# Performance work log

Hardware: AMD Instinct MI355X
Metric: run time of the kernel (lower is better)

Reference implementation:

```python
import math
import jax, jax.numpy as jnp
import numpy as np

N_HEADS = 16


def setup_inputs() -> dict:
    key = jax.random.key(0)
    qkv = jax.random.normal(key, (4, 3072, 2048), dtype=jnp.float32)
    return {"qkv": qkv}


def reference(qkv) -> jnp.ndarray:
    bs, width, length = qkv.shape
    assert width % (3 * N_HEADS) == 0
    ch = width // (3 * N_HEADS)
    # [bs*H, 3*ch, T] -> q, k, v each [bs*H, ch, T]
    qkv_r = qkv.reshape(bs * N_HEADS, 3 * ch, length)
    q, k, v = qkv_r[:, :ch], qkv_r[:, ch:2 * ch], qkv_r[:, 2 * ch:]
    scale = 1.0 / math.sqrt(math.sqrt(ch))
    # scores: [bs*H, T, T]
    weight = jnp.einsum('bct,bcs->bts', q * scale, k * scale)
    weight = jax.nn.softmax(weight.astype(jnp.float32), axis=-1).astype(weight.dtype)
    a = jnp.einsum('bts,bcs->bct', weight, v)  # [bs*H, ch, T]
    return a.reshape(bs, N_HEADS * ch, length)
```

## Files before the change

### kernel.cpp

```cpp
#include <hip/hip_runtime.h>
#include <hip/hip_bf16.h>
#include <cstdint>
#include <cstddef>

typedef short bf16x8 __attribute__((ext_vector_type(8)));
typedef float f32x16 __attribute__((ext_vector_type(16)));
typedef unsigned int uint2v __attribute__((ext_vector_type(2)));

#if __has_builtin(__builtin_amdgcn_exp2f)
#define EXP2F(x) __builtin_amdgcn_exp2f(x)
#else
#define EXP2F(x) exp2f(x)
#endif

#define QSCALE 0.18033688011112043f

__device__ __forceinline__ short f2bf(float f) {
  union { __hip_bfloat16 b; short s; } u;
  u.b = __float2bfloat16(f);
  return u.s;
}

__device__ __forceinline__ unsigned int fbits(float f) {
  union { float f; unsigned int u; } x; x.f = f; return x.u;
}
__device__ __forceinline__ float bfloat(unsigned int u) {
  union { unsigned int u; float f; } x; x.u = u; return x.f;
}

__device__ __forceinline__ unsigned int pkbf(float a, float b) {
  return ((fbits(a) + 0x8000u) >> 16) | ((fbits(b) + 0x8000u) & 0xFFFF0000u);
}

__device__ __forceinline__ float fmax_x32(float v) {
  const uint2v r = __builtin_amdgcn_permlane32_swap(fbits(v), fbits(v),
                                                    false, false);
  return fmaxf(bfloat(r[0]), bfloat(r[1]));
}
__device__ __forceinline__ float fadd_x32(float v) {
  const uint2v r = __builtin_amdgcn_permlane32_swap(fbits(v), fbits(v),
                                                    false, false);
  return bfloat(r[0]) + bfloat(r[1]);
}

__device__ __forceinline__ void gload16(const short* g, char* l) {
  __builtin_amdgcn_global_load_lds(
      (const __attribute__((address_space(1))) void*)g,
      (__attribute__((address_space(3))) void*)l, 16, 0, 0);
}

__global__ __launch_bounds__(256, 4) void qkv_prep_kernel(
    const float* __restrict__ qkv, short* __restrict__ Kt,
    short* __restrict__ Vb) {
  const int bh = blockIdx.x >> 5;
  const int s0 = (blockIdx.x & 31) << 6;
  const int tid = threadIdx.x;
  const int row = tid >> 2;
  const int part = tid & 3;
  __shared__ float lds[64 * 65];

  const size_t qb = (size_t)bh * (192 * 2048);

  {
    const float* src = qkv + qb + (size_t)(64 + row) * 2048 + s0 + part * 16;
#pragma unroll
    for (int k4 = 0; k4 < 4; ++k4) {
      float4 v = ((const float4*)src)[k4];
      float* p = &lds[row * 65 + part * 16 + k4 * 4];
      p[0] = v.x; p[1] = v.y; p[2] = v.z; p[3] = v.w;
    }
  }
  __syncthreads();
  {
    bf16x8 o0, o1;
#pragma unroll
    for (int k = 0; k < 8; ++k) o0[k] = f2bf(lds[(part * 16 + k) * 65 + row]);
#pragma unroll
    for (int k = 0; k < 8; ++k) o1[k] = f2bf(lds[(part * 16 + 8 + k) * 65 + row]);
    short* dst = Kt + ((size_t)bh * 2048 + s0 + row) * 64 + part * 16;
    *(bf16x8*)dst = o0;
    *(bf16x8*)(dst + 8) = o1;
  }
  {
    const float* src = qkv + qb + (size_t)(128 + row) * 2048 + s0 + part * 16;
    float a[16];
#pragma unroll
    for (int k4 = 0; k4 < 4; ++k4) {
      float4 v = ((const float4*)src)[k4];
      a[k4 * 4 + 0] = v.x; a[k4 * 4 + 1] = v.y;
      a[k4 * 4 + 2] = v.z; a[k4 * 4 + 3] = v.w;
    }
    bf16x8 o0, o1;
#pragma unroll
    for (int k = 0; k < 8; ++k) { o0[k] = f2bf(a[k]); o1[k] = f2bf(a[8 + k]); }
    short* dst = Vb + ((size_t)bh * 64 + row) * 2048 + s0 + part * 16;
    *(bf16x8*)dst = o0;
    *(bf16x8*)(dst + 8) = o1;
  }
}

__global__ __launch_bounds__(512, 4) void attn32_kernel(
    const float* __restrict__ qkv, const short* __restrict__ Kt,
    const short* __restrict__ Vb, float* __restrict__ out) {
  const int bid = blockIdx.x;
  const int vid = (bid & 7) * 64 + (bid >> 3);
  const int bh = vid >> 3;
  const int tblk = vid & 7;
  const int tid = threadIdx.x;
  const int wv = tid >> 6;
  const int lane = tid & 63;
  const int tl = lane & 31;
  const int hi = lane >> 5;
  const int t0w = tblk * 256 + wv * 32;

  __shared__ __align__(16) char smem[32768];

  const size_t qb = (size_t)bh * (192 * 2048);
  bf16x8 qf[4];
#pragma unroll
  for (int kc = 0; kc < 4; ++kc) {
#pragma unroll
    for (int j = 0; j < 8; ++j) {
      const int c = kc * 16 + hi * 8 + j;
      qf[kc][j] = f2bf(qkv[qb + (size_t)c * 2048 + t0w + tl] * QSCALE);
    }
  }

  f32x16 zv;
#pragma unroll
  for (int r = 0; r < 16; ++r) zv[r] = 0.f;

  f32x16 acc[2];
#pragma unroll
  for (int cb = 0; cb < 2; ++cb) acc[cb] = zv;

  float mrun = -1e30f;
  float lsum = 0.f;

  const int rsw = (tl & 7) * 16;
  int off[2][4];
#pragma unroll
  for (int x = 0; x < 2; ++x)
#pragma unroll
    for (int j = 0; j < 4; ++j)
      off[x][j] = (x * 32 + tl) * 128 + ((j * 32 + hi * 16) ^ rsw);

  const int srow = tid >> 3;
  const int sl = tid & 7;
  const short* kg = Kt + (size_t)bh * (2048 * 64) + (size_t)srow * 64 +
                    ((sl ^ (srow & 7)) * 8);
  const short* vg = Vb + ((size_t)bh * 64 + srow) * 2048 +
                    ((sl ^ (srow & 7)) * 8);
  const int ldb = wv * 1024;

  gload16(kg, smem + ldb);
  gload16(vg, smem + 8192 + ldb);

#pragma unroll 2
  for (int ch = 0; ch < 32; ++ch) {
    char* const Kls = smem + (ch & 1) * 16384;
    char* const Vls = Kls + 8192;

    __syncthreads();

    if (ch < 31) {
      char* const Knx = smem + ((ch + 1) & 1) * 16384;
      gload16(kg + (size_t)(ch + 1) * 4096, Knx + ldb);
      gload16(vg + (ch + 1) * 64, Knx + 8192 + ldb);
    }

    f32x16 lg[2];
#pragma unroll
    for (int st = 0; st < 2; ++st) {
      bf16x8 ka = *(const bf16x8*)(Kls + off[st][0]);
      lg[st] = __builtin_amdgcn_mfma_f32_32x32x16_bf16(ka, qf[0], zv, 0, 0, 0);
#pragma unroll
      for (int kc = 1; kc < 4; ++kc) {
        ka = *(const bf16x8*)(Kls + off[st][kc]);
        lg[st] = __builtin_amdgcn_mfma_f32_32x32x16_bf16(ka, qf[kc], lg[st],
                                                         0, 0, 0);
      }
    }

    float w[11];
#pragma unroll
    for (int i = 0; i < 5; ++i)
      w[i] = fmaxf(fmaxf(lg[0][3 * i], lg[0][3 * i + 1]), lg[0][3 * i + 2]);
    w[5] = fmaxf(fmaxf(lg[0][15], lg[1][0]), lg[1][1]);
#pragma unroll
    for (int i = 0; i < 4; ++i)
      w[6 + i] = fmaxf(fmaxf(lg[1][3 * i + 2], lg[1][3 * i + 3]),
                       lg[1][3 * i + 4]);
    w[10] = fmaxf(lg[1][14], lg[1][15]);
    const float x0 = fmaxf(fmaxf(w[0], w[1]), w[2]);
    const float x1 = fmaxf(fmaxf(w[3], w[4]), w[5]);
    const float x2 = fmaxf(fmaxf(w[6], w[7]), w[8]);
    const float x3 = fmaxf(w[9], w[10]);
    float cm = fmax_x32(fmaxf(fmaxf(x0, x1), fmaxf(x2, x3)));
    if (!__all(cm <= mrun + 8.0f)) {
      const float nm = fmaxf(mrun, cm);
      const float fac = EXP2F(mrun - nm);
      mrun = nm;
      lsum *= fac;
#pragma unroll
      for (int cb = 0; cb < 2; ++cb)
#pragma unroll
        for (int r = 0; r < 16; ++r) acc[cb][r] *= fac;
    }

    float ps = 0.f;
#pragma unroll
    for (int st = 0; st < 2; ++st) {
#pragma unroll
      for (int r = 0; r < 16; ++r) lg[st][r] = EXP2F(lg[st][r] - mrun);
#pragma unroll
      for (int r = 0; r < 8; ++r) ps += lg[st][2 * r] + lg[st][2 * r + 1];
    }
    lsum += ps;

    bf16x8 pa[4];
#pragma unroll
    for (int st = 0; st < 2; ++st) {
#pragma unroll
      for (int kl = 0; kl < 2; ++kl) {
        const unsigned int p0a = pkbf(lg[st][8 * kl + 0], lg[st][8 * kl + 1]);
        const unsigned int p0b = pkbf(lg[st][8 * kl + 2], lg[st][8 * kl + 3]);
        const unsigned int p1a = pkbf(lg[st][8 * kl + 4], lg[st][8 * kl + 5]);
        const unsigned int p1b = pkbf(lg[st][8 * kl + 6], lg[st][8 * kl + 7]);
        const unsigned int sa = hi ? p0a : p1a;
        const unsigned int sb = hi ? p0b : p1b;
        const unsigned int ra = __shfl_xor(sa, 32);
        const unsigned int rb = __shfl_xor(sb, 32);
        union { unsigned int w[4]; bf16x8 v; } u;
        u.w[0] = hi ? ra : p0a;
        u.w[1] = hi ? rb : p0b;
        u.w[2] = hi ? p1a : ra;
        u.w[3] = hi ? p1b : rb;
        pa[st * 2 + kl] = u.v;
      }
    }

#pragma unroll
    for (int cb = 0; cb < 2; ++cb) {
#pragma unroll
      for (int ks = 0; ks < 4; ++ks) {
        const bf16x8 vb = *(const bf16x8*)(Vls + off[cb][ks]);
        acc[cb] = __builtin_amdgcn_mfma_f32_32x32x16_bf16(vb, pa[ks], acc[cb],
                                                          0, 0, 0);
      }
    }
  }

  const float ls = fadd_x32(lsum);
  const float inv = 1.0f / ls;
#pragma unroll
  for (int cb = 0; cb < 2; ++cb) {
#pragma unroll
    for (int r = 0; r < 16; ++r) {
      const int c = cb * 32 + (r & 3) + 8 * (r >> 2) + 4 * hi;
      out[((size_t)bh * 64 + c) * 2048 + t0w + tl] = acc[cb][r] * inv;
    }
  }
}

extern "C" void kernel_launch(void* const* d_in, const int* in_sizes, int n_in,
                              void* d_out, int out_size, void* d_ws,
                              size_t ws_size, hipStream_t stream) {
  (void)in_sizes; (void)n_in; (void)out_size;
  const float* qkv = (const float*)d_in[0];
  float* out = (float*)d_out;
  const size_t kv_elems = (size_t)64 * 2048 * 64;
  if (ws_size < kv_elems * 2 * sizeof(short)) return;
  short* Kt = (short*)d_ws;
  short* Vb = Kt + kv_elems;
  hipLaunchKernelGGL(qkv_prep_kernel, dim3(2048), dim3(256), 0, stream,
                     qkv, Kt, Vb);
  hipLaunchKernelGGL(attn32_kernel, dim3(512), dim3(512), 0, stream,
                     qkv, Kt, Vb, out);
}
```

Baseline: 116.9 us.

## Drop LDS staging and read K/V fragments directly from global memory

Removes the double-buffered LDS staging of K and V tiles, along with its async global-to-LDS loads and per-chunk barriers. Each wave now loads its MFMA operand fragments straight from global memory, relying on L1/L2 for reuse across waves. Blocks shrink from 8 to 4 waves, covering 128 query positions instead of 256, and the grid doubles to keep the total work the same. This removes barrier stalls and LDS traffic, but every wave now fetches K/V through cache, which duplicates global/L2 traffic and exposes load latency without explicit prefetching.

```diff
diff --git a/kernel.cpp b/kernel.cpp
--- a/kernel.cpp
+++ b/kernel.cpp
@@ -41,12 +41,6 @@
   const uint2v r = __builtin_amdgcn_permlane32_swap(fbits(v), fbits(v),
                                                     false, false);
   return bfloat(r[0]) + bfloat(r[1]);
-}
-
-__device__ __forceinline__ void gload16(const short* g, char* l) {
-  __builtin_amdgcn_global_load_lds(
-      (const __attribute__((address_space(1))) void*)g,
-      (__attribute__((address_space(3))) void*)l, 16, 0, 0);
 }
 
 __global__ __launch_bounds__(256, 4) void qkv_prep_kernel(
@@ -99,21 +93,19 @@
   }
 }
 
-__global__ __launch_bounds__(512, 4) void attn32_kernel(
+__global__ __launch_bounds__(256, 4) void attn32_kernel(
     const float* __restrict__ qkv, const short* __restrict__ Kt,
     const short* __restrict__ Vb, float* __restrict__ out) {
   const int bid = blockIdx.x;
-  const int vid = (bid & 7) * 64 + (bid >> 3);
-  const int bh = vid >> 3;
-  const int tblk = vid & 7;
+  const int vid = (bid & 7) * 128 + (bid >> 3);
+  const int bh = vid >> 4;
+  const int tblk = vid & 15;
   const int tid = threadIdx.x;
   const int wv = tid >> 6;
   const int lane = tid & 63;
   const int tl = lane & 31;
   const int hi = lane >> 5;
-  const int t0w = tblk * 256 + wv * 32;
-
-  __shared__ __align__(16) char smem[32768];
+  const int t0w = tblk * 128 + wv * 32;
 
   const size_t qb = (size_t)bh * (192 * 2048);
   bf16x8 qf[4];
@@ -137,46 +129,24 @@
   float mrun = -1e30f;
   float lsum = 0.f;
 
-  const int rsw = (tl & 7) * 16;
-  int off[2][4];
-#pragma unroll
-  for (int x = 0; x < 2; ++x)
-#pragma unroll
-    for (int j = 0; j < 4; ++j)
-      off[x][j] = (x * 32 + tl) * 128 + ((j * 32 + hi * 16) ^ rsw);
-
-  const int srow = tid >> 3;
-  const int sl = tid & 7;
-  const short* kg = Kt + (size_t)bh * (2048 * 64) + (size_t)srow * 64 +
-                    ((sl ^ (srow & 7)) * 8);
-  const short* vg = Vb + ((size_t)bh * 64 + srow) * 2048 +
-                    ((sl ^ (srow & 7)) * 8);
-  const int ldb = wv * 1024;
-
-  gload16(kg, smem + ldb);
-  gload16(vg, smem + 8192 + ldb);
-
-#pragma unroll 2
+  const short* kp0 = Kt + (size_t)bh * (2048 * 64) + (size_t)tl * 64 + hi * 8;
+  const short* kp1 = kp0 + 32 * 64;
+  const short* vp0 = Vb + ((size_t)bh * 64 + tl) * 2048 + hi * 8;
+  const short* vp1 = vp0 + (size_t)32 * 2048;
+
   for (int ch = 0; ch < 32; ++ch) {
-    char* const Kls = smem + (ch & 1) * 16384;
-    char* const Vls = Kls + 8192;
-
-    __syncthreads();
-
-    if (ch < 31) {
-      char* const Knx = smem + ((ch + 1) & 1) * 16384;
-      gload16(kg + (size_t)(ch + 1) * 4096, Knx + ldb);
-      gload16(vg + (ch + 1) * 64, Knx + 8192 + ldb);
-    }
+    const size_t kofs = (size_t)ch * 4096;
+    const int sofs = ch * 64;
 
     f32x16 lg[2];
 #pragma unroll
     for (int st = 0; st < 2; ++st) {
-      bf16x8 ka = *(const bf16x8*)(Kls + off[st][0]);
+      const short* kp = st ? kp1 : kp0;
+      bf16x8 ka = *(const bf16x8*)(kp + kofs);
       lg[st] = __builtin_amdgcn_mfma_f32_32x32x16_bf16(ka, qf[0], zv, 0, 0, 0);
 #pragma unroll
       for (int kc = 1; kc < 4; ++kc) {
-        ka = *(const bf16x8*)(Kls + off[st][kc]);
+        ka = *(const bf16x8*)(kp + kofs + kc * 16);
         lg[st] = __builtin_amdgcn_mfma_f32_32x32x16_bf16(ka, qf[kc], lg[st],
                                                          0, 0, 0);
       }
@@ -242,9 +212,10 @@
 
 #pragma unroll
     for (int cb = 0; cb < 2; ++cb) {
+      const short* vp = cb ? vp1 : vp0;
 #pragma unroll
       for (int ks = 0; ks < 4; ++ks) {
-        const bf16x8 vb = *(const bf16x8*)(Vls + off[cb][ks]);
+        const bf16x8 vb = *(const bf16x8*)(vp + sofs + ks * 16);
         acc[cb] = __builtin_amdgcn_mfma_f32_32x32x16_bf16(vb, pa[ks], acc[cb],
                                                           0, 0, 0);
       }
@@ -275,6 +246,6 @@
   short* Vb = Kt + kv_elems;
   hipLaunchKernelGGL(qkv_prep_kernel, dim3(2048), dim3(256), 0, stream,
                      qkv, Kt, Vb);
-  hipLaunchKernelGGL(attn32_kernel, dim3(512), dim3(512), 0, stream,
+  hipLaunchKernelGGL(attn32_kernel, dim3(1024), dim3(256), 0, stream,
                      qkv, Kt, Vb, out);
 }
```

New measurement: 253.7 us. 117% more time.

## Process two key/value chunks per barrier with doubled LDS staging

Applied to the files above, without the earlier changes.

Each loop iteration now loads two 64-key K and V chunks into a 64KB double-buffered LDS region, so there are 16 barriers instead of 32. Both QK^T products are issued back to back before the two softmax/PV stages, giving the scheduler more independent MFMA work to overlap with the exp math. In exchange, LDS use doubles to 64KB per block, which may cut the number of resident blocks per CU below the launch-bounds target of 4. Register pressure also rises from holding two score tiles at once.

```diff
diff --git a/kernel.cpp b/kernel.cpp
--- a/kernel.cpp
+++ b/kernel.cpp
@@ -113,7 +113,7 @@
   const int hi = lane >> 5;
   const int t0w = tblk * 256 + wv * 32;
 
-  __shared__ __align__(16) char smem[32768];
+  __shared__ __align__(16) char smem[65536];
 
   const size_t qb = (size_t)bh * (192 * 2048);
   bf16x8 qf[4];
@@ -153,100 +153,123 @@
                     ((sl ^ (srow & 7)) * 8);
   const int ldb = wv * 1024;
 
-  gload16(kg, smem + ldb);
-  gload16(vg, smem + 8192 + ldb);
-
-#pragma unroll 2
-  for (int ch = 0; ch < 32; ++ch) {
-    char* const Kls = smem + (ch & 1) * 16384;
-    char* const Vls = Kls + 8192;
+  gload16(kg, smem + 0 * 8192 + ldb);
+  gload16(kg + 4096, smem + 1 * 8192 + ldb);
+  gload16(vg, smem + 2 * 8192 + ldb);
+  gload16(vg + 64, smem + 3 * 8192 + ldb);
+
+  for (int p = 0; p < 16; ++p) {
+    char* const base = smem + (p & 1) * 32768;
 
     __syncthreads();
 
-    if (ch < 31) {
-      char* const Knx = smem + ((ch + 1) & 1) * 16384;
-      gload16(kg + (size_t)(ch + 1) * 4096, Knx + ldb);
-      gload16(vg + (ch + 1) * 64, Knx + 8192 + ldb);
-    }
-
-    f32x16 lg[2];
+    if (p < 15) {
+      char* const nb = smem + ((p + 1) & 1) * 32768;
+      const size_t k0 = (size_t)(2 * p + 2) * 4096;
+      const int v0 = (2 * p + 2) * 64;
+      gload16(kg + k0, nb + 0 * 8192 + ldb);
+      gload16(kg + k0 + 4096, nb + 1 * 8192 + ldb);
+      gload16(vg + v0, nb + 2 * 8192 + ldb);
+      gload16(vg + v0 + 64, nb + 3 * 8192 + ldb);
+    }
+
+    f32x16 lgA[2], lgB[2];
 #pragma unroll
     for (int st = 0; st < 2; ++st) {
+      const char* Kls = base;
       bf16x8 ka = *(const bf16x8*)(Kls + off[st][0]);
-      lg[st] = __builtin_amdgcn_mfma_f32_32x32x16_bf16(ka, qf[0], zv, 0, 0, 0);
+      lgA[st] = __builtin_amdgcn_mfma_f32_32x32x16_bf16(ka, qf[0], zv, 0, 0, 0);
 #pragma unroll
       for (int kc = 1; kc < 4; ++kc) {
         ka = *(const bf16x8*)(Kls + off[st][kc]);
-        lg[st] = __builtin_amdgcn_mfma_f32_32x32x16_bf16(ka, qf[kc], lg[st],
-                                                         0, 0, 0);
-      }
-    }
-
-    float w[11];
-#pragma unroll
-    for (int i = 0; i < 5; ++i)
-      w[i] = fmaxf(fmaxf(lg[0][3 * i], lg[0][3 * i + 1]), lg[0][3 * i + 2]);
-    w[5] = fmaxf(fmaxf(lg[0][15], lg[1][0]), lg[1][1]);
-#pragma unroll
-    for (int i = 0; i < 4; ++i)
-      w[6 + i] = fmaxf(fmaxf(lg[1][3 * i + 2], lg[1][3 * i + 3]),
-                       lg[1][3 * i + 4]);
-    w[10] = fmaxf(lg[1][14], lg[1][15]);
-    const float x0 = fmaxf(fmaxf(w[0], w[1]), w[2]);
-    const float x1 = fmaxf(fmaxf(w[3], w[4]), w[5]);
-    const float x2 = fmaxf(fmaxf(w[6], w[7]), w[8]);
-    const float x3 = fmaxf(w[9], w[10]);
-    float cm = fmax_x32(fmaxf(fmaxf(x0, x1), fmaxf(x2, x3)));
-    if (!__all(cm <= mrun + 8.0f)) {
-      const float nm = fmaxf(mrun, cm);
-      const float fac = EXP2F(mrun - nm);
-      mrun = nm;
-      lsum *= fac;
-#pragma unroll
-      for (int cb = 0; cb < 2; ++cb)
-#pragma unroll
-        for (int r = 0; r < 16; ++r) acc[cb][r] *= fac;
-    }
-
-    float ps = 0.f;
+        lgA[st] = __builtin_amdgcn_mfma_f32_32x32x16_bf16(ka, qf[kc], lgA[st],
+                                                          0, 0, 0);
+      }
+    }
 #pragma unroll
     for (int st = 0; st < 2; ++st) {
-#pragma unroll
-      for (int r = 0; r < 16; ++r) lg[st][r] = EXP2F(lg[st][r] - mrun);
-#pragma unroll
-      for (int r = 0; r < 8; ++r) ps += lg[st][2 * r] + lg[st][2 * r + 1];
-    }
-    lsum += ps;
-
-    bf16x8 pa[4];
-#pragma unroll
-    for (int st = 0; st < 2; ++st) {
-#pragma unroll
-      for (int kl = 0; kl < 2; ++kl) {
-        const unsigned int p0a = pkbf(lg[st][8 * kl + 0], lg[st][8 * kl + 1]);
-        const unsigned int p0b = pkbf(lg[st][8 * kl + 2], lg[st][8 * kl + 3]);
-        const unsigned int p1a = pkbf(lg[st][8 * kl + 4], lg[st][8 * kl + 5]);
-        const unsigned int p1b = pkbf(lg[st][8 * kl + 6], lg[st][8 * kl + 7]);
-        const unsigned int sa = hi ? p0a : p1a;
-        const unsigned int sb = hi ? p0b : p1b;
-        const unsigned int ra = __shfl_xor(sa, 32);
-        const unsigned int rb = __shfl_xor(sb, 32);
-        union { unsigned int w[4]; bf16x8 v; } u;
-        u.w[0] = hi ? ra : p0a;
-        u.w[1] = hi ? rb : p0b;
-        u.w[2] = hi ? p1a : ra;
-        u.w[3] = hi ? p1b : rb;
-        pa[st * 2 + kl] = u.v;
-      }
-    }
-
-#pragma unroll
-    for (int cb = 0; cb < 2; ++cb) {
-#pragma unroll
-      for (int ks = 0; ks < 4; ++ks) {
-        const bf16x8 vb = *(const bf16x8*)(Vls + off[cb][ks]);
-        acc[cb] = __builtin_amdgcn_mfma_f32_32x32x16_bf16(vb, pa[ks], acc[cb],
+      const char* Kls = base + 8192;
+      bf16x8 ka = *(const bf16x8*)(Kls + off[st][0]);
+      lgB[st] = __builtin_amdgcn_mfma_f32_32x32x16_bf16(ka, qf[0], zv, 0, 0, 0);
+#pragma unroll
+      for (int kc = 1; kc < 4; ++kc) {
+        ka = *(const bf16x8*)(Kls + off[st][kc]);
+        lgB[st] = __builtin_amdgcn_mfma_f32_32x32x16_bf16(ka, qf[kc], lgB[st],
                                                           0, 0, 0);
+      }
+    }
+
+#pragma unroll
+    for (int sub = 0; sub < 2; ++sub) {
+      f32x16* lg = sub ? lgB : lgA;
+      const char* Vls = base + 16384 + sub * 8192;
+
+      float w[11];
+#pragma unroll
+      for (int i = 0; i < 5; ++i)
+        w[i] = fmaxf(fmaxf(lg[0][3 * i], lg[0][3 * i + 1]), lg[0][3 * i + 2]);
+      w[5] = fmaxf(fmaxf(lg[0][15], lg[1][0]), lg[1][1]);
+#pragma unroll
+      for (int i = 0; i < 4; ++i)
+        w[6 + i] = fmaxf(fmaxf(lg[1][3 * i + 2], lg[1][3 * i + 3]),
+                         lg[1][3 * i + 4]);
+      w[10] = fmaxf(lg[1][14], lg[1][15]);
+      const float x0 = fmaxf(fmaxf(w[0], w[1]), w[2]);
+      const float x1 = fmaxf(fmaxf(w[3], w[4]), w[5]);
+      const float x2 = fmaxf(fmaxf(w[6], w[7]), w[8]);
+      const float x3 = fmaxf(w[9], w[10]);
+      float cm = fmax_x32(fmaxf(fmaxf(x0, x1), fmaxf(x2, x3)));
+      if (!__all(cm <= mrun + 8.0f)) {
+        const float nm = fmaxf(mrun, cm);
+        const float fac = EXP2F(mrun - nm);
+        mrun = nm;
+        lsum *= fac;
+#pragma unroll
+        for (int cb = 0; cb < 2; ++cb)
+#pragma unroll
+          for (int r = 0; r < 16; ++r) acc[cb][r] *= fac;
+      }
+
+      float ps = 0.f;
+#pragma unroll
+      for (int st = 0; st < 2; ++st) {
+#pragma unroll
+        for (int r = 0; r < 16; ++r) lg[st][r] = EXP2F(lg[st][r] - mrun);
+#pragma unroll
+        for (int r = 0; r < 8; ++r) ps += lg[st][2 * r] + lg[st][2 * r + 1];
+      }
+      lsum += ps;
+
+      bf16x8 pa[4];
+#pragma unroll
+      for (int st = 0; st < 2; ++st) {
+#pragma unroll
+        for (int kl = 0; kl < 2; ++kl) {
+          const unsigned int p0a = pkbf(lg[st][8 * kl + 0], lg[st][8 * kl + 1]);
+          const unsigned int p0b = pkbf(lg[st][8 * kl + 2], lg[st][8 * kl + 3]);
+          const unsigned int p1a = pkbf(lg[st][8 * kl + 4], lg[st][8 * kl + 5]);
+          const unsigned int p1b = pkbf(lg[st][8 * kl + 6], lg[st][8 * kl + 7]);
+          const unsigned int sa = hi ? p0a : p1a;
+          const unsigned int sb = hi ? p0b : p1b;
+          const unsigned int ra = __shfl_xor(sa, 32);
+          const unsigned int rb = __shfl_xor(sb, 32);
+          union { unsigned int w[4]; bf16x8 v; } u;
+          u.w[0] = hi ? ra : p0a;
+          u.w[1] = hi ? rb : p0b;
+          u.w[2] = hi ? p1a : ra;
+          u.w[3] = hi ? p1b : rb;
+          pa[st * 2 + kl] = u.v;
+        }
+      }
+
+#pragma unroll
+      for (int cb = 0; cb < 2; ++cb) {
+#pragma unroll
+        for (int ks = 0; ks < 4; ++ks) {
+          const bf16x8 vb = *(const bf16x8*)(Vls + off[cb][ks]);
+          acc[cb] = __builtin_amdgcn_mfma_f32_32x32x16_bf16(vb, pa[ks],
+                                                            acc[cb], 0, 0, 0);
+        }
       }
     }
   }
```

New measurement: 135.9 us. +16.3%, slower.
